# Kernel optimization log

Hardware: AMD Instinct MI355X
Metric: run time of the kernel (lower is better)

## Reference

```python
import jax, jax.numpy as jnp
import numpy as np

TOP_K = 2

def setup_inputs() -> dict:
    key = jax.random.key(0)
    k1, k2 = jax.random.split(key)
    D, E = 4096, 64
    hidden_states = jax.random.normal(k1, (2, 8192, D), dtype=jnp.float32)
    W = jax.random.normal(k2, (E, D), dtype=jnp.float32) / np.sqrt(D)
    b = jnp.zeros((E,), dtype=jnp.float32)
    return {"hidden_states": hidden_states, "W": W, "b": b}

def reference(hidden_states, W, b):
    # gate: logits [B, S, E]
    logits = jnp.einsum('bsd,ed->bse', hidden_states, W) + b
    scores = jax.nn.softmax(logits, axis=-1)
    top_k_values, top_k_indices = jax.lax.top_k(scores, TOP_K)
    return ((top_k_indices, top_k_values), scores)
```

## Files before the change

kernel.cpp:

```cpp
#include <hip/hip_runtime.h>
#include <math.h>

#define D_DIM 4096
#define E_DIM 64
#define TM 64
#define BK 64
#define KSPLIT 4
#define KPART (D_DIM / KSPLIT)
#define KCH (KPART / BK)
#define TP 68
#define LP 65

__global__ __launch_bounds__(256, 4) void router_gemm(
    const float* __restrict__ hs,
    const float* __restrict__ W,
    float* __restrict__ logits,
    int nTok)
{
    __shared__ float hsT[BK * TP];
    __shared__ float wT [BK * TP];

    const int tid   = threadIdx.x;
    const int part  = blockIdx.x & (KSPLIT - 1);
    const int tBase = (blockIdx.x >> 2) * TM;
    const int kBase = part * KPART;

    const int ty = tid >> 4;
    const int tx = tid & 15;

    const int dq = tid & 15;
    const int r  = tid >> 4;

    float4 ph[4], pw[4];
    float acc[4][4];
    #pragma unroll
    for (int i = 0; i < 4; ++i)
        #pragma unroll
        for (int j = 0; j < 4; ++j)
            acc[i][j] = 0.f;

    const float* hsB = hs + (size_t)tBase * D_DIM + kBase;
    const float* WB  = W + kBase;

    auto g_load = [&](int c) {
        const int d = c * BK + dq * 4;
        #pragma unroll
        for (int p = 0; p < 4; ++p) {
            const int row = p * 16 + r;
            ph[p] = *(const float4*)&hsB[(size_t)row * D_DIM + d];
            pw[p] = *(const float4*)&WB [(size_t)row * D_DIM + d];
        }
    };

    auto l_store = [&]() {
        #pragma unroll
        for (int p = 0; p < 4; ++p) {
            const int row = p * 16 + r;
            #pragma unroll
            for (int i = 0; i < 4; ++i) {
                hsT[(dq * 4 + i) * TP + row] = ((const float*)&ph[p])[i];
                wT [(dq * 4 + i) * TP + row] = ((const float*)&pw[p])[i];
            }
        }
    };

    auto compute = [&]() {
        #pragma unroll
        for (int kk = 0; kk < BK; ++kk) {
            const float4 a = *(const float4*)&hsT[kk * TP + ty * 4];
            const float4 w = *(const float4*)&wT [kk * TP + tx * 4];
            const float av[4] = {a.x, a.y, a.z, a.w};
            const float wv[4] = {w.x, w.y, w.z, w.w};
            #pragma unroll
            for (int i = 0; i < 4; ++i)
                #pragma unroll
                for (int j = 0; j < 4; ++j)
                    acc[i][j] = fmaf(av[i], wv[j], acc[i][j]);
        }
    };

    g_load(0);
    l_store();
    __syncthreads();
    #pragma unroll 1
    for (int c = 0; c < KCH - 1; ++c) {
        g_load(c + 1);
        compute();
        __syncthreads();
        l_store();
        __syncthreads();
    }
    compute();

    #pragma unroll
    for (int i = 0; i < 4; ++i) {
        const size_t rowOff = (size_t)(tBase + ty * 4 + i) * E_DIM + tx * 4;
        #pragma unroll
        for (int j = 0; j < 4; ++j)
            unsafeAtomicAdd(&logits[rowOff + j], acc[i][j]);
    }
}

__global__ __launch_bounds__(256, 4) void router_epilogue(
    const float* __restrict__ bias,
    float* __restrict__ out,
    int nTok)
{
    __shared__ float lg[64 * LP];
    __shared__ float s_m[64];
    __shared__ float s_inv[64];

    const int tid   = threadIdx.x;
    const int tBase = blockIdx.x * 64;

    float* out_idx = out;
    float* out_val = out + (size_t)nTok * 2;
    float* sc      = out + (size_t)nTok * 4;

    #pragma unroll
    for (int p = 0; p < 4; ++p) {
        const int f = p * 1024 + tid * 4;
        const float4 v  = *(const float4*)&sc[(size_t)tBase * E_DIM + f];
        const int t = f >> 6, e = f & 63;
        const float4 bb = *(const float4*)&bias[e];
        lg[t * LP + e + 0] = v.x + bb.x;
        lg[t * LP + e + 1] = v.y + bb.y;
        lg[t * LP + e + 2] = v.z + bb.z;
        lg[t * LP + e + 3] = v.w + bb.w;
    }
    __syncthreads();

    if (tid < 64) {
        const int t = tid;
        const float* row = &lg[t * LP];
        float m = row[0];
        #pragma unroll
        for (int e = 1; e < E_DIM; ++e) m = fmaxf(m, row[e]);
        float sum = 0.f;
        float b1 = -INFINITY, b2 = -INFINITY;
        int i1 = 0, i2 = 0;
        for (int e = 0; e < E_DIM; ++e) {
            const float l = row[e];
            sum += __expf(l - m);
            if (l > b1)      { b2 = b1; i2 = i1; b1 = l; i1 = e; }
            else if (l > b2) { b2 = l; i2 = e; }
        }
        const float inv = 1.f / sum;
        s_m[t]   = m;
        s_inv[t] = inv;
        const size_t gt = (size_t)(tBase + t);
        out_idx[gt * 2 + 0] = (float)i1;
        out_idx[gt * 2 + 1] = (float)i2;
        out_val[gt * 2 + 0] = __expf(b1 - m) * inv;
        out_val[gt * 2 + 1] = __expf(b2 - m) * inv;
    }
    __syncthreads();

    const int e  = tid & 63;
    const int tq = tid >> 6;
    #pragma unroll
    for (int p = 0; p < 16; ++p) {
        const int t = p * 4 + tq;
        sc[(size_t)(tBase + t) * E_DIM + e] =
            __expf(lg[t * LP + e] - s_m[t]) * s_inv[t];
    }
}

extern "C" void kernel_launch(void* const* d_in, const int* in_sizes, int n_in,
                              void* d_out, int out_size, void* d_ws, size_t ws_size,
                              hipStream_t stream) {
    const float* hs = (const float*)d_in[0];
    const float* W  = (const float*)d_in[1];
    const float* b  = (const float*)d_in[2];
    float* out = (float*)d_out;
    const int nTok = in_sizes[0] / D_DIM;

    float* logits = out + (size_t)nTok * 4;
    hipMemsetAsync(logits, 0, (size_t)nTok * E_DIM * sizeof(float), stream);

    dim3 g1(nTok / TM * KSPLIT), b1(256);
    router_gemm<<<g1, b1, 0, stream>>>(hs, W, logits, nTok);

    dim3 g2(nTok / 64), b2(256);
    router_epilogue<<<g2, b2, 0, stream>>>(b, out, nTok);
}
```

Measured before the change: 446.1 us.

## Use split-bf16 MFMA for router GEMM and shuffle-based softmax epilogue

Replaces the FP32 FMA tiled GEMM with bf16 MFMA 16x16x32 instructions, splitting each fp32 operand into three bf16 parts and doing six products to approximate fp32 accuracy. W is staged in shared memory as three bf16 planes, while hidden-state rows are loaded straight into registers and split on the fly. The epilogue now uses four lanes per token with xor-shuffles for the top-2 and softmax reductions, replacing the single-thread serial loops and the shared-memory staging. This trades extra split arithmetic and six MFMAs per k-step for matrix-core throughput, with a small precision difference from true fp32.

```diff
diff --git a/kernel.cpp b/kernel.cpp
--- a/kernel.cpp
+++ b/kernel.cpp
@@ -4,12 +4,37 @@
 #define D_DIM 4096
 #define E_DIM 64
 #define TM 64
-#define BK 64
 #define KSPLIT 4
 #define KPART (D_DIM / KSPLIT)
-#define KCH (KPART / BK)
-#define TP 68
-#define LP 65
+#define CHK 64
+#define NCH (KPART / CHK)
+#define WROW 72
+
+typedef __attribute__((ext_vector_type(8))) short bf16x8;
+typedef __attribute__((ext_vector_type(4))) float f32x4;
+
+__device__ inline void split3(const f32x4 a0, const f32x4 a1,
+                              bf16x8& fh, bf16x8& fm, bf16x8& fl) {
+    uint uh[8], um[8], ul[8];
+    float f[8] = {a0[0], a0[1], a0[2], a0[3], a1[0], a1[1], a1[2], a1[3]};
+    #pragma unroll
+    for (int j = 0; j < 8; ++j) {
+        const uint u = __float_as_uint(f[j]);
+        const uint h = u & 0xFFFF0000u;
+        const float r = f[j] - __uint_as_float(h);
+        const uint m = __float_as_uint(r) & 0xFFFF0000u;
+        const float r2 = r - __uint_as_float(m);
+        uh[j] = h; um[j] = m; ul[j] = __float_as_uint(r2);
+    }
+    union { bf16x8 v; uint u[4]; } H, M, L;
+    #pragma unroll
+    for (int j = 0; j < 4; ++j) {
+        H.u[j] = (uh[2*j] >> 16) | (uh[2*j+1] & 0xFFFF0000u);
+        M.u[j] = (um[2*j] >> 16) | (um[2*j+1] & 0xFFFF0000u);
+        L.u[j] = (ul[2*j] >> 16) | (ul[2*j+1] & 0xFFFF0000u);
+    }
+    fh = H.v; fm = M.v; fl = L.v;
+}
 
 __global__ __launch_bounds__(256, 4) void router_gemm(
     const float* __restrict__ hs,
@@ -17,88 +42,101 @@
     float* __restrict__ logits,
     int nTok)
 {
-    __shared__ float hsT[BK * TP];
-    __shared__ float wT [BK * TP];
-
-    const int tid   = threadIdx.x;
-    const int part  = blockIdx.x & (KSPLIT - 1);
-    const int tBase = (blockIdx.x >> 2) * TM;
-    const int kBase = part * KPART;
-
-    const int ty = tid >> 4;
-    const int tx = tid & 15;
-
-    const int dq = tid & 15;
-    const int r  = tid >> 4;
-
-    float4 ph[4], pw[4];
-    float acc[4][4];
-    #pragma unroll
-    for (int i = 0; i < 4; ++i)
+    __shared__ short wsh[E_DIM * WROW];
+    __shared__ short wsm[E_DIM * WROW];
+    __shared__ short wsl[E_DIM * WROW];
+
+    const int tid  = threadIdx.x;
+    const int lane = tid & 63;
+    const int wv   = tid >> 6;
+    const int part = blockIdx.x & (KSPLIT - 1);
+    const int tb   = (blockIdx.x >> 2) * TM;
+    const int kb   = part * KPART;
+
+    const int l15 = lane & 15;
+    const int lq  = lane >> 4;
+
+    const float* aptr = hs + (size_t)(tb + wv * 16 + l15) * D_DIM + kb + lq * 8;
+    const int we = tid >> 2;
+    const int wq = tid & 3;
+    const float* wptr = W + (size_t)we * D_DIM + kb + wq * 16;
+
+    f32x4 acc[4];
+    #pragma unroll
+    for (int t = 0; t < 4; ++t) acc[t] = (f32x4){0.f, 0.f, 0.f, 0.f};
+
+    f32x4 ca[4], pa[4], wr[4];
+
+    auto loadA = [&](int ch, f32x4* dst) {
+        const float* p = aptr + ch * CHK;
+        dst[0] = *(const f32x4*)(p);
+        dst[1] = *(const f32x4*)(p + 4);
+        dst[2] = *(const f32x4*)(p + 32);
+        dst[3] = *(const f32x4*)(p + 36);
+    };
+    auto loadW = [&](int ch) {
+        const float* p = wptr + ch * CHK;
+        wr[0] = *(const f32x4*)(p);
+        wr[1] = *(const f32x4*)(p + 4);
+        wr[2] = *(const f32x4*)(p + 8);
+        wr[3] = *(const f32x4*)(p + 12);
+    };
+    auto storeW = [&]() {
+        bf16x8 h0, m0, l0, h1, m1, l1;
+        split3(wr[0], wr[1], h0, m0, l0);
+        split3(wr[2], wr[3], h1, m1, l1);
+        const int base = we * WROW + wq * 16;
+        *(bf16x8*)&wsh[base] = h0;  *(bf16x8*)&wsh[base + 8] = h1;
+        *(bf16x8*)&wsm[base] = m0;  *(bf16x8*)&wsm[base + 8] = m1;
+        *(bf16x8*)&wsl[base] = l0;  *(bf16x8*)&wsl[base + 8] = l1;
+    };
+    auto compute = [&](const f32x4* a) {
         #pragma unroll
-        for (int j = 0; j < 4; ++j)
-            acc[i][j] = 0.f;
-
-    const float* hsB = hs + (size_t)tBase * D_DIM + kBase;
-    const float* WB  = W + kBase;
-
-    auto g_load = [&](int c) {
-        const int d = c * BK + dq * 4;
-        #pragma unroll
-        for (int p = 0; p < 4; ++p) {
-            const int row = p * 16 + r;
-            ph[p] = *(const float4*)&hsB[(size_t)row * D_DIM + d];
-            pw[p] = *(const float4*)&WB [(size_t)row * D_DIM + d];
-        }
-    };
-
-    auto l_store = [&]() {
-        #pragma unroll
-        for (int p = 0; p < 4; ++p) {
-            const int row = p * 16 + r;
+        for (int s = 0; s < 2; ++s) {
+            bf16x8 ah, am, al;
+            split3(a[2 * s], a[2 * s + 1], ah, am, al);
+            const int koff = s * 32 + lq * 8;
             #pragma unroll
-            for (int i = 0; i < 4; ++i) {
-                hsT[(dq * 4 + i) * TP + row] = ((const float*)&ph[p])[i];
-                wT [(dq * 4 + i) * TP + row] = ((const float*)&pw[p])[i];
+            for (int t = 0; t < 4; ++t) {
+                const int rb = (t * 16 + l15) * WROW + koff;
+                const bf16x8 bh = *(const bf16x8*)&wsh[rb];
+                const bf16x8 bm = *(const bf16x8*)&wsm[rb];
+                const bf16x8 bl = *(const bf16x8*)&wsl[rb];
+                acc[t] = __builtin_amdgcn_mfma_f32_16x16x32_bf16(ah, bh, acc[t], 0, 0, 0);
+                acc[t] = __builtin_amdgcn_mfma_f32_16x16x32_bf16(ah, bm, acc[t], 0, 0, 0);
+                acc[t] = __builtin_amdgcn_mfma_f32_16x16x32_bf16(am, bh, acc[t], 0, 0, 0);
+                acc[t] = __builtin_amdgcn_mfma_f32_16x16x32_bf16(ah, bl, acc[t], 0, 0, 0);
+                acc[t] = __builtin_amdgcn_mfma_f32_16x16x32_bf16(al, bh, acc[t], 0, 0, 0);
+                acc[t] = __builtin_amdgcn_mfma_f32_16x16x32_bf16(am, bm, acc[t], 0, 0, 0);
             }
         }
     };
 
-    auto compute = [&]() {
-        #pragma unroll
-        for (int kk = 0; kk < BK; ++kk) {
-            const float4 a = *(const float4*)&hsT[kk * TP + ty * 4];
-            const float4 w = *(const float4*)&wT [kk * TP + tx * 4];
-            const float av[4] = {a.x, a.y, a.z, a.w};
-            const float wv[4] = {w.x, w.y, w.z, w.w};
-            #pragma unroll
-            for (int i = 0; i < 4; ++i)
-                #pragma unroll
-                for (int j = 0; j < 4; ++j)
-                    acc[i][j] = fmaf(av[i], wv[j], acc[i][j]);
-        }
-    };
-
-    g_load(0);
-    l_store();
+    loadA(0, ca);
+    loadW(0);
+    storeW();
     __syncthreads();
     #pragma unroll 1
-    for (int c = 0; c < KCH - 1; ++c) {
-        g_load(c + 1);
-        compute();
-        __syncthreads();
-        l_store();
-        __syncthreads();
-    }
-    compute();
-
-    #pragma unroll
-    for (int i = 0; i < 4; ++i) {
-        const size_t rowOff = (size_t)(tBase + ty * 4 + i) * E_DIM + tx * 4;
+    for (int ch = 0; ch < NCH; ++ch) {
+        const bool last = (ch == NCH - 1);
+        if (!last) loadA(ch + 1, pa);
+        compute(ca);
+        if (!last) {
+            loadW(ch + 1);
+            __syncthreads();
+            storeW();
+            __syncthreads();
+            #pragma unroll
+            for (int i = 0; i < 4; ++i) ca[i] = pa[i];
+        }
+    }
+
+    float* dst = logits + (size_t)(tb + wv * 16) * E_DIM;
+    #pragma unroll
+    for (int t = 0; t < 4; ++t)
         #pragma unroll
-        for (int j = 0; j < 4; ++j)
-            unsafeAtomicAdd(&logits[rowOff + j], acc[i][j]);
-    }
+        for (int r = 0; r < 4; ++r)
+            unsafeAtomicAdd(&dst[(size_t)(lq * 4 + r) * E_DIM + t * 16 + l15], acc[t][r]);
 }
 
 __global__ __launch_bounds__(256, 4) void router_epilogue(
@@ -106,63 +144,74 @@
     float* __restrict__ out,
     int nTok)
 {
-    __shared__ float lg[64 * LP];
-    __shared__ float s_m[64];
-    __shared__ float s_inv[64];
-
-    const int tid   = threadIdx.x;
-    const int tBase = blockIdx.x * 64;
+    const int tid = threadIdx.x;
+    const int tok = blockIdx.x * 64 + (tid >> 2);
+    const int g   = tid & 3;
 
     float* out_idx = out;
     float* out_val = out + (size_t)nTok * 2;
     float* sc      = out + (size_t)nTok * 4;
 
-    #pragma unroll
-    for (int p = 0; p < 4; ++p) {
-        const int f = p * 1024 + tid * 4;
-        const float4 v  = *(const float4*)&sc[(size_t)tBase * E_DIM + f];
-        const int t = f >> 6, e = f & 63;
-        const float4 bb = *(const float4*)&bias[e];
-        lg[t * LP + e + 0] = v.x + bb.x;
-        lg[t * LP + e + 1] = v.y + bb.y;
-        lg[t * LP + e + 2] = v.z + bb.z;
-        lg[t * LP + e + 3] = v.w + bb.w;
-    }
-    __syncthreads();
-
-    if (tid < 64) {
-        const int t = tid;
-        const float* row = &lg[t * LP];
-        float m = row[0];
-        #pragma unroll
-        for (int e = 1; e < E_DIM; ++e) m = fmaxf(m, row[e]);
-        float sum = 0.f;
-        float b1 = -INFINITY, b2 = -INFINITY;
-        int i1 = 0, i2 = 0;
-        for (int e = 0; e < E_DIM; ++e) {
-            const float l = row[e];
-            sum += __expf(l - m);
-            if (l > b1)      { b2 = b1; i2 = i1; b1 = l; i1 = e; }
-            else if (l > b2) { b2 = l; i2 = e; }
+    float* src = sc + (size_t)tok * E_DIM + g * 16;
+    float v[16];
+    #pragma unroll
+    for (int j = 0; j < 4; ++j) {
+        const f32x4 x = *(const f32x4*)(src + j * 4);
+        const f32x4 b = *(const f32x4*)(bias + g * 16 + j * 4);
+        v[j * 4 + 0] = x[0] + b[0];
+        v[j * 4 + 1] = x[1] + b[1];
+        v[j * 4 + 2] = x[2] + b[2];
+        v[j * 4 + 3] = x[3] + b[3];
+    }
+
+    float b1 = -INFINITY, b2 = -INFINITY;
+    int i1 = 0, i2 = 0;
+    #pragma unroll
+    for (int j = 0; j < 16; ++j) {
+        const float x = v[j];
+        const int idx = g * 16 + j;
+        if (x > b1)      { b2 = b1; i2 = i1; b1 = x; i1 = idx; }
+        else if (x > b2) { b2 = x; i2 = idx; }
+    }
+    #pragma unroll
+    for (int d = 1; d <= 2; d <<= 1) {
+        const float ob1 = __shfl_xor(b1, d);
+        const int   oi1 = __shfl_xor(i1, d);
+        const float ob2 = __shfl_xor(b2, d);
+        const int   oi2 = __shfl_xor(i2, d);
+        if (ob1 > b1 || (ob1 == b1 && oi1 < i1)) {
+            if (b1 > ob2 || (b1 == ob2 && i1 < oi2)) { b2 = b1; i2 = i1; }
+            else                                     { b2 = ob2; i2 = oi2; }
+            b1 = ob1; i1 = oi1;
+        } else {
+            if (ob1 > b2 || (ob1 == b2 && oi1 < i2)) { b2 = ob1; i2 = oi1; }
         }
-        const float inv = 1.f / sum;
-        s_m[t]   = m;
-        s_inv[t] = inv;
-        const size_t gt = (size_t)(tBase + t);
-        out_idx[gt * 2 + 0] = (float)i1;
-        out_idx[gt * 2 + 1] = (float)i2;
-        out_val[gt * 2 + 0] = __expf(b1 - m) * inv;
-        out_val[gt * 2 + 1] = __expf(b2 - m) * inv;
-    }
-    __syncthreads();
-
-    const int e  = tid & 63;
-    const int tq = tid >> 6;
-    #pragma unroll
-    for (int p = 0; p < 16; ++p) {
-        const int t = p * 4 + tq;
-        sc[(size_t)(tBase + t) * E_DIM + e] =
-            __expf(lg[t * LP + e] - s_m[t]) * s_inv[t];
+    }
+    const float m = b1;
+
+    float e[16];
+    float s = 0.f;
+    #pragma unroll
+    for (int j = 0; j < 16; ++j) { e[j] = __expf(v[j] - m); s += e[j]; }
+    s += __shfl_xor(s, 1);
+    s += __shfl_xor(s, 2);
+    const float inv = 1.f / s;
+
+    if (g == 0) {
+        out_idx[(size_t)tok * 2 + 0] = (float)i1;
+        out_idx[(size_t)tok * 2 + 1] = (float)i2;
+        out_val[(size_t)tok * 2 + 0] = inv;
+        out_val[(size_t)tok * 2 + 1] = __expf(b2 - m) * inv;
+    }
+
+    #pragma unroll
+    for (int j = 0; j < 4; ++j) {
+        f32x4 o;
+        o[0] = e[j * 4 + 0] * inv;
+        o[1] = e[j * 4 + 1] * inv;
+        o[2] = e[j * 4 + 2] * inv;
+        o[3] = e[j * 4 + 3] * inv;
+        *(f32x4*)(src + j * 4) = o;
     }
 }
 
```

Measured after the change: 385.1 us. -13.7%, faster.
